# Kernel optimization log

Measured on AMD Instinct MI355X. Metric: run time of the kernel, lower is better.

The kernel has to match this reference:

```python
import jax, jax.numpy as jnp
import numpy as np

D_MODEL = 1024
NUM_HEADS = 16
HEAD_DIM = D_MODEL // NUM_HEADS
B, S = 2, 2048


def setup_inputs() -> dict:
    key = jax.random.key(0)
    ks = jax.random.split(key, 6)
    scale = 0.02
    return {
        "x": jax.random.normal(ks[0], (B, S, D_MODEL), dtype=jnp.float32),
        "mask": jax.random.normal(ks[1], (S, S), dtype=jnp.float32),
        "Wqkv": jax.random.normal(ks[2], (D_MODEL, 3 * D_MODEL), dtype=jnp.float32) * scale,
        "bqkv": jax.random.normal(ks[3], (3 * D_MODEL,), dtype=jnp.float32) * scale,
        "Wout": jax.random.normal(ks[4], (D_MODEL, D_MODEL), dtype=jnp.float32) * scale,
        "bout": jax.random.normal(ks[5], (D_MODEL,), dtype=jnp.float32) * scale,
    }


def reference(x, mask, Wqkv, bqkv, Wout, bout):
    b, s, d = x.shape
    h, hd = NUM_HEADS, HEAD_DIM
    qkv = x @ Wqkv + bqkv                              # [b, s, 3d]
    qkv = qkv.reshape(b, s, h, 3 * hd).transpose(0, 2, 1, 3)  # [b, h, s, 3hd]
    q, k, v = jnp.split(qkv, 3, axis=-1)               # each [b, h, s, hd]
    scaled = jnp.einsum("bhqd,bhkd->bhqk", q, k) / jnp.sqrt(jnp.float32(hd))
    scaled = scaled + mask                             # mask [s, s] broadcasts
    attn = jax.nn.softmax(scaled, axis=-1)
    values = jnp.einsum("bhqk,bhkd->bhqd", attn, v)    # [b, h, s, hd]
    values = values.transpose(0, 2, 1, 3).reshape(b, s, d)
    return values @ Wout + bout
```

## Files before the change

### kernel.cpp

```cpp
#include <hip/hip_runtime.h>
#include <hip/hip_bf16.h>

#define D_MODEL 1024
#define NH 16
#define HD 64
#define BATCH 2
#define SEQ 2048
#define M_TOTAL (BATCH*SEQ)

typedef _Float16 f16;
typedef _Float16 half8 __attribute__((ext_vector_type(8)));
typedef _Float16 half4v __attribute__((ext_vector_type(4)));
typedef float floatx4 __attribute__((ext_vector_type(4)));

__device__ inline void gload_lds16(const void* g, void* l) {
    __builtin_amdgcn_global_load_lds(
        (const __attribute__((address_space(1))) unsigned int*)g,
        (__attribute__((address_space(3))) unsigned int*)l, 16, 0, 0);
}

__global__ void cvt_f32_f16(const float* __restrict__ src, f16* __restrict__ dst, int n4) {
    int i = blockIdx.x * blockDim.x + threadIdx.x;
    if (i < n4) {
        float4 v = ((const float4*)src)[i];
        half4v o = { (f16)v.x, (f16)v.y, (f16)v.z, (f16)v.w };
        *(half4v*)(dst + (long)i * 4) = o;
    }
}

__global__ void exp_cvt(const float* __restrict__ src, f16* __restrict__ dst, int n4) {
    int i = blockIdx.x * blockDim.x + threadIdx.x;
    if (i < n4) {
        float4 v = ((const float4*)src)[i];
        half4v o = { (f16)__expf(v.x), (f16)__expf(v.y), (f16)__expf(v.z), (f16)__expf(v.w) };
        *(half4v*)(dst + (long)i * 4) = o;
    }
}

__global__ void transpose_cvt(const float* __restrict__ src, f16* __restrict__ dst, int R, int C) {
    __shared__ float tile[32][33];
    int tx = threadIdx.x;
    int ty = threadIdx.y;
    int c0 = blockIdx.x * 32;
    int r0 = blockIdx.y * 32;
    for (int yy = 0; yy < 32; yy += 8)
        tile[ty + yy][tx] = src[(long)(r0 + ty + yy) * C + c0 + tx];
    __syncthreads();
    for (int yy = 0; yy < 32; yy += 8)
        dst[(long)(c0 + ty + yy) * R + r0 + tx] = (f16)tile[tx][ty + yy];
}

template<int MODE, int TN>
__global__ __launch_bounds__(256) void gemm_mfma(
    const f16* __restrict__ A, const f16* __restrict__ BT,
    const float* __restrict__ bias,
    f16* __restrict__ Qh, f16* __restrict__ Kh, f16* __restrict__ Vtg,
    float* __restrict__ out, int Kdim)
{
    constexpr int NF = TN / 32;
    __shared__ f16 Ah[128 * 64];
    __shared__ f16 Bh[TN * 64];
    int tid  = threadIdx.x;
    int wid  = tid >> 6;
    int lane = tid & 63;
    int quad = lane >> 4;
    int l16  = lane & 15;
    int m0 = blockIdx.y * 128;
    int n0 = blockIdx.x * TN;
    int mrow = (wid >> 1) * 64;
    int ncol = (wid & 1) * (TN / 2);
    int grow = lane >> 3;
    int gchunk = (lane & 7) ^ (grow & 7);
    int sw0 = ((quad)     ^ (l16 & 7)) * 8;
    int sw1 = ((quad + 4) ^ (l16 & 7)) * 8;

    floatx4 acc[4][NF];
    #pragma unroll
    for (int mb = 0; mb < 4; mb++)
        #pragma unroll
        for (int nb = 0; nb < NF; nb++) acc[mb][nb] = (floatx4){0.f, 0.f, 0.f, 0.f};

    const f16* Abase = A + (long)m0 * Kdim;
    const f16* Bbase = BT + (long)n0 * Kdim;

    for (int k0 = 0; k0 < Kdim; k0 += 64) {
        #pragma unroll
        for (int j = 0; j < 4; j++) {
            int r = j * 32 + wid * 8 + grow;
            gload_lds16(Abase + (long)r * Kdim + k0 + gchunk * 8, &Ah[(j * 32 + wid * 8) * 64]);
        }
        #pragma unroll
        for (int j = 0; j < TN / 32; j++) {
            int r = j * 32 + wid * 8 + grow;
            gload_lds16(Bbase + (long)r * Kdim + k0 + gchunk * 8, &Bh[(j * 32 + wid * 8) * 64]);
        }
        __syncthreads();
        #pragma unroll
        for (int h = 0; h < 2; h++) {
            int sw = h ? sw1 : sw0;
            half8 af[4];
            #pragma unroll
            for (int mb = 0; mb < 4; mb++)
                af[mb] = *(const half8*)&Ah[(mrow + mb * 16 + l16) * 64 + sw];
            #pragma unroll
            for (int nb = 0; nb < NF; nb++) {
                half8 bf = *(const half8*)&Bh[(ncol + nb * 16 + l16) * 64 + sw];
                #pragma unroll
                for (int mb = 0; mb < 4; mb++)
                    acc[mb][nb] = __builtin_amdgcn_mfma_f32_16x16x32_f16(af[mb], bf, acc[mb][nb], 0, 0, 0);
            }
        }
        __syncthreads();
    }

    #pragma unroll
    for (int nb = 0; nb < NF; nb++) {
        int n = n0 + ncol + nb * 16 + l16;
        float bv = bias[n];
        int head = 0, t = 0, d = 0;
        if (MODE == 0) { head = n / 192; int rem = n % 192; t = rem / 64; d = rem % 64; }
        #pragma unroll
        for (int mb = 0; mb < 4; mb++) {
            int mbase = m0 + mrow + mb * 16 + quad * 4;
            if (MODE == 0) {
                int b = mbase >> 11;
                int s = mbase & 2047;
                long bh = b * NH + head;
                if (t == 2) {
                    half4v pack;
                    #pragma unroll
                    for (int r = 0; r < 4; r++) pack[r] = (f16)(acc[mb][nb][r] + bv);
                    *(half4v*)&Vtg[(bh * HD + d) * SEQ + s] = pack;
                } else if (t == 0) {
                    #pragma unroll
                    for (int r = 0; r < 4; r++)
                        Qh[(bh * SEQ + s + r) * HD + d] = (f16)((acc[mb][nb][r] + bv) * 0.125f);
                } else {
                    #pragma unroll
                    for (int r = 0; r < 4; r++)
                        Kh[(bh * SEQ + s + r) * HD + d] = (f16)(acc[mb][nb][r] + bv);
                }
            } else {
                #pragma unroll
                for (int r = 0; r < 4; r++)
                    out[(long)(mbase + r) * D_MODEL + n] = acc[mb][nb][r] + bv;
            }
        }
    }
}

__global__ __launch_bounds__(512) void attn(
    const f16* __restrict__ Qh, const f16* __restrict__ Kh, const f16* __restrict__ Vtg,
    const f16* __restrict__ E, f16* __restrict__ valh)
{
    __shared__ f16 Kl[2][64 * 64];
    __shared__ f16 Vt[2][64 * 64];
    __shared__ f16 Pl[8][16 * 68];
    int tid  = threadIdx.x;
    int wid  = tid >> 6;
    int lane = tid & 63;
    int quad = lane >> 4;
    int l16  = lane & 15;
    int bh = blockIdx.y;
    int b  = bh >> 4;
    int h  = bh & 15;
    int qblk = blockIdx.x * 128;
    int q0 = qblk + wid * 16;

    int wrow = wid * 8 + (lane >> 3);
    int kchunk = (lane & 7) ^ (wrow & 7);
    int sw0 = ((quad)     ^ (l16 & 7)) * 8;
    int sw1 = ((quad + 4) ^ (l16 & 7)) * 8;

    const f16* Qbase = Qh + ((long)bh * SEQ + q0) * HD;
    half8 qf[2];
    #pragma unroll
    for (int c = 0; c < 2; c++)
        qf[c] = *(const half8*)&Qbase[(long)l16 * HD + c * 32 + quad * 8];

    floatx4 Of[4];
    float sums[4];
    #pragma unroll
    for (int nb = 0; nb < 4; nb++) Of[nb] = (floatx4){0.f, 0.f, 0.f, 0.f};
    #pragma unroll
    for (int r = 0; r < 4; r++) sums[r] = 0.f;

    const f16* Kb = Kh + (long)bh * SEQ * HD;
    const f16* Vb = Vtg + (long)bh * HD * SEQ;
    const f16* Eb = E + (long)qblk * SEQ;

    auto stage = [&](int buf, int k0) {
        gload_lds16(Kb + (long)(k0 + wrow) * HD + kchunk * 8, &Kl[buf][(wid * 8) * 64]);
        gload_lds16(Vb + (long)wrow * SEQ + k0 + kchunk * 8, &Vt[buf][(wid * 8) * 64]);
    };
    auto loadE = [&](f16 (&ef)[4][4], int k0) {
        #pragma unroll
        for (int r = 0; r < 4; r++) {
            const f16* Erow = Eb + (long)(wid * 16 + quad * 4 + r) * SEQ + k0 + l16;
            #pragma unroll
            for (int kb = 0; kb < 4; kb++) ef[r][kb] = Erow[kb * 16];
        }
    };

    f16 efA[4][4], efB[4][4];
    stage(0, 0);
    loadE(efA, 0);
    __syncthreads();

    auto iter = [&](const int buf, f16 (&efC)[4][4], f16 (&efN)[4][4], int k0) {
        bool notlast = (k0 + 64 < SEQ);
        if (notlast) stage(buf ^ 1, k0 + 64);

        floatx4 sc[4];
        #pragma unroll
        for (int kb = 0; kb < 4; kb++) {
            half8 kf0 = *(const half8*)&Kl[buf][(kb * 16 + l16) * 64 + sw0];
            half8 kf1 = *(const half8*)&Kl[buf][(kb * 16 + l16) * 64 + sw1];
            floatx4 s = (floatx4){0.f, 0.f, 0.f, 0.f};
            s = __builtin_amdgcn_mfma_f32_16x16x32_f16(qf[0], kf0, s, 0, 0, 0);
            s = __builtin_amdgcn_mfma_f32_16x16x32_f16(qf[1], kf1, s, 0, 0, 0);
            sc[kb] = s;
        }

        #pragma unroll
        for (int kb = 0; kb < 4; kb++)
            #pragma unroll
            for (int r = 0; r < 4; r++) {
                float p = (float)efC[r][kb] * __expf(sc[kb][r]);
                sums[r] += p;
                Pl[wid][(quad * 4 + r) * 68 + kb * 16 + l16] = (f16)p;
            }

        if (notlast) loadE(efN, k0 + 64);

        half8 pf0 = *(const half8*)&Pl[wid][l16 * 68 + quad * 8];
        half8 pf1 = *(const half8*)&Pl[wid][l16 * 68 + 32 + quad * 8];

        #pragma unroll
        for (int nb = 0; nb < 4; nb++) {
            half8 vf0 = *(const half8*)&Vt[buf][(nb * 16 + l16) * 64 + sw0];
            half8 vf1 = *(const half8*)&Vt[buf][(nb * 16 + l16) * 64 + sw1];
            Of[nb] = __builtin_amdgcn_mfma_f32_16x16x32_f16(pf0, vf0, Of[nb], 0, 0, 0);
            Of[nb] = __builtin_amdgcn_mfma_f32_16x16x32_f16(pf1, vf1, Of[nb], 0, 0, 0);
        }

        __syncthreads();
    };

    for (int k0 = 0; k0 < SEQ; k0 += 128) {
        iter(0, efA, efB, k0);
        iter(1, efB, efA, k0 + 64);
    }

    float rinv[4];
    #pragma unroll
    for (int r = 0; r < 4; r++) {
        float s = sums[r];
        s += __shfl_xor(s, 1);
        s += __shfl_xor(s, 2);
        s += __shfl_xor(s, 4);
        s += __shfl_xor(s, 8);
        rinv[r] = 1.f / s;
    }

    #pragma unroll
    for (int nb = 0; nb < 4; nb++)
        #pragma unroll
        for (int r = 0; r < 4; r++) {
            int q = q0 + quad * 4 + r;
            int d = nb * 16 + l16;
            valh[((long)(b * SEQ + q)) * D_MODEL + h * HD + d] = (f16)(Of[nb][r] * rinv[r]);
        }
}

extern "C" void kernel_launch(void* const* d_in, const int* in_sizes, int n_in,
                              void* d_out, int out_size, void* d_ws, size_t ws_size,
                              hipStream_t stream) {
    const float* x    = (const float*)d_in[0];
    const float* mask = (const float*)d_in[1];
    const float* Wqkv = (const float*)d_in[2];
    const float* bqkv = (const float*)d_in[3];
    const float* Wout = (const float*)d_in[4];
    const float* bout = (const float*)d_in[5];
    float* out = (float*)d_out;

    char* ws = (char*)d_ws;
    f16* xh    = (f16*)(ws + 0);
    f16* E     = (f16*)(ws + 0);
    f16* WqkvT = (f16*)(ws + 8388608);
    f16* WoutT = (f16*)(ws + 14680064);
    f16* Qh    = (f16*)(ws + 16777216);
    f16* Kh    = (f16*)(ws + 25165824);
    f16* Vtg   = (f16*)(ws + 33554432);
    f16* valh  = (f16*)(ws + 41943040);

    cvt_f32_f16<<<4096, 256, 0, stream>>>(x, xh, M_TOTAL * D_MODEL / 4);
    transpose_cvt<<<dim3(96, 32), dim3(32, 8), 0, stream>>>(Wqkv, WqkvT, 1024, 3072);
    transpose_cvt<<<dim3(32, 32), dim3(32, 8), 0, stream>>>(Wout, WoutT, 1024, 1024);
    gemm_mfma<0, 128><<<dim3(24, 32), 256, 0, stream>>>(xh, WqkvT, bqkv, Qh, Kh, Vtg, nullptr, 1024);
    exp_cvt<<<4096, 256, 0, stream>>>(mask, E, SEQ * SEQ / 4);
    attn<<<dim3(16, 32), 512, 0, stream>>>(Qh, Kh, Vtg, E, valh);
    gemm_mfma<1, 64><<<dim3(16, 32), 256, 0, stream>>>(valh, WoutT, bout, nullptr, nullptr, nullptr, out, 1024);
}
```

Measured before the change: 219.7 us.

## Fold mask into exp2 argument, sum rows via MFMA, remap blocks per XCD

```diff
diff --git a/kernel.cpp b/kernel.cpp
--- a/kernel.cpp
+++ b/kernel.cpp
@@ -13,6 +13,12 @@
 typedef _Float16 half4v __attribute__((ext_vector_type(4)));
 typedef float floatx4 __attribute__((ext_vector_type(4)));
 
+#if __has_builtin(__builtin_amdgcn_exp2f)
+#define EXP2(x) __builtin_amdgcn_exp2f(x)
+#else
+#define EXP2(x) __expf(0.6931471805599453f * (x))
+#endif
+
 __device__ inline void gload_lds16(const void* g, void* l) {
     __builtin_amdgcn_global_load_lds(
         (const __attribute__((address_space(1))) unsigned int*)g,
@@ -28,11 +34,12 @@
     }
 }
 
-__global__ void exp_cvt(const float* __restrict__ src, f16* __restrict__ dst, int n4) {
+__global__ void l2scale_cvt(const float* __restrict__ src, f16* __restrict__ dst, int n4) {
     int i = blockIdx.x * blockDim.x + threadIdx.x;
     if (i < n4) {
         float4 v = ((const float4*)src)[i];
-        half4v o = { (f16)__expf(v.x), (f16)__expf(v.y), (f16)__expf(v.z), (f16)__expf(v.w) };
+        const float L2E = 1.44269504f;
+        half4v o = { (f16)(v.x * L2E), (f16)(v.y * L2E), (f16)(v.z * L2E), (f16)(v.w * L2E) };
         *(half4v*)(dst + (long)i * 4) = o;
     }
 }
@@ -134,7 +141,7 @@
                 } else if (t == 0) {
                     #pragma unroll
                     for (int r = 0; r < 4; r++)
-                        Qh[(bh * SEQ + s + r) * HD + d] = (f16)((acc[mb][nb][r] + bv) * 0.125f);
+                        Qh[(bh * SEQ + s + r) * HD + d] = (f16)((acc[mb][nb][r] + bv) * 0.18033688f);
                 } else {
                     #pragma unroll
                     for (int r = 0; r < 4; r++)
@@ -161,10 +168,15 @@
     int lane = tid & 63;
     int quad = lane >> 4;
     int l16  = lane & 15;
-    int bh = blockIdx.y;
+
+    int id   = blockIdx.y * 16 + blockIdx.x;
+    int xcd  = id & 7;
+    int slot = id >> 3;
+    int bh   = ((xcd & 3) << 3) | (slot >> 3);
+    int qx   = ((xcd >> 2) << 3) | (slot & 7);
     int b  = bh >> 4;
     int h  = bh & 15;
-    int qblk = blockIdx.x * 128;
+    int qblk = qx * 128;
     int q0 = qblk + wid * 16;
 
     int wrow = wid * 8 + (lane >> 3);
@@ -178,12 +190,14 @@
     for (int c = 0; c < 2; c++)
         qf[c] = *(const half8*)&Qbase[(long)l16 * HD + c * 32 + quad * 8];
 
+    half8 onesv;
+    #pragma unroll
+    for (int j = 0; j < 8; j++) onesv[j] = (f16)1.0f;
+
     floatx4 Of[4];
-    float sums[4];
+    floatx4 ssum = (floatx4){0.f, 0.f, 0.f, 0.f};
     #pragma unroll
     for (int nb = 0; nb < 4; nb++) Of[nb] = (floatx4){0.f, 0.f, 0.f, 0.f};
-    #pragma unroll
-    for (int r = 0; r < 4; r++) sums[r] = 0.f;
 
     const f16* Kb = Kh + (long)bh * SEQ * HD;
     const f16* Vb = Vtg + (long)bh * HD * SEQ;
@@ -193,25 +207,24 @@
         gload_lds16(Kb + (long)(k0 + wrow) * HD + kchunk * 8, &Kl[buf][(wid * 8) * 64]);
         gload_lds16(Vb + (long)wrow * SEQ + k0 + kchunk * 8, &Vt[buf][(wid * 8) * 64]);
     };
-    auto loadE = [&](f16 (&ef)[4][4], int k0) {
+
+    stage(0, 0);
+    __syncthreads();
+
+    auto iter = [&](const int buf, int k0) {
+        bool notlast = (k0 + 64 < SEQ);
+        if (notlast) stage(buf ^ 1, k0 + 64);
+
+        f16 ef[4][4];
         #pragma unroll
         for (int r = 0; r < 4; r++) {
             const f16* Erow = Eb + (long)(wid * 16 + quad * 4 + r) * SEQ + k0 + l16;
             #pragma unroll
             for (int kb = 0; kb < 4; kb++) ef[r][kb] = Erow[kb * 16];
         }
-    };
-
-    f16 efA[4][4], efB[4][4];
-    stage(0, 0);
-    loadE(efA, 0);
-    __syncthreads();
-
-    auto iter = [&](const int buf, f16 (&efC)[4][4], f16 (&efN)[4][4], int k0) {
-        bool notlast = (k0 + 64 < SEQ);
-        if (notlast) stage(buf ^ 1, k0 + 64);
 
         floatx4 sc[4];
+        __builtin_amdgcn_s_setprio(1);
         #pragma unroll
         for (int kb = 0; kb < 4; kb++) {
             half8 kf0 = *(const half8*)&Kl[buf][(kb * 16 + l16) * 64 + sw0];
@@ -221,21 +234,22 @@
             s = __builtin_amdgcn_mfma_f32_16x16x32_f16(qf[1], kf1, s, 0, 0, 0);
             sc[kb] = s;
         }
+        __builtin_amdgcn_s_setprio(0);
 
         #pragma unroll
         for (int kb = 0; kb < 4; kb++)
             #pragma unroll
             for (int r = 0; r < 4; r++) {
-                float p = (float)efC[r][kb] * __expf(sc[kb][r]);
-                sums[r] += p;
+                float p = EXP2(sc[kb][r] + (float)ef[r][kb]);
                 Pl[wid][(quad * 4 + r) * 68 + kb * 16 + l16] = (f16)p;
             }
 
-        if (notlast) loadE(efN, k0 + 64);
-
         half8 pf0 = *(const half8*)&Pl[wid][l16 * 68 + quad * 8];
         half8 pf1 = *(const half8*)&Pl[wid][l16 * 68 + 32 + quad * 8];
 
+        __builtin_amdgcn_s_setprio(1);
+        ssum = __builtin_amdgcn_mfma_f32_16x16x32_f16(pf0, onesv, ssum, 0, 0, 0);
+        ssum = __builtin_amdgcn_mfma_f32_16x16x32_f16(pf1, onesv, ssum, 0, 0, 0);
         #pragma unroll
         for (int nb = 0; nb < 4; nb++) {
             half8 vf0 = *(const half8*)&Vt[buf][(nb * 16 + l16) * 64 + sw0];
@@ -243,25 +257,19 @@
             Of[nb] = __builtin_amdgcn_mfma_f32_16x16x32_f16(pf0, vf0, Of[nb], 0, 0, 0);
             Of[nb] = __builtin_amdgcn_mfma_f32_16x16x32_f16(pf1, vf1, Of[nb], 0, 0, 0);
         }
+        __builtin_amdgcn_s_setprio(0);
 
         __syncthreads();
     };
 
     for (int k0 = 0; k0 < SEQ; k0 += 128) {
-        iter(0, efA, efB, k0);
-        iter(1, efB, efA, k0 + 64);
+        iter(0, k0);
+        iter(1, k0 + 64);
     }
 
     float rinv[4];
     #pragma unroll
-    for (int r = 0; r < 4; r++) {
-        float s = sums[r];
-        s += __shfl_xor(s, 1);
-        s += __shfl_xor(s, 2);
-        s += __shfl_xor(s, 4);
-        s += __shfl_xor(s, 8);
-        rinv[r] = 1.f / s;
-    }
+    for (int r = 0; r < 4; r++) rinv[r] = 1.f / ssum[r];
 
     #pragma unroll
     for (int nb = 0; nb < 4; nb++)
@@ -298,7 +306,7 @@
     transpose_cvt<<<dim3(96, 32), dim3(32, 8), 0, stream>>>(Wqkv, WqkvT, 1024, 3072);
     transpose_cvt<<<dim3(32, 32), dim3(32, 8), 0, stream>>>(Wout, WoutT, 1024, 1024);
     gemm_mfma<0, 128><<<dim3(24, 32), 256, 0, stream>>>(xh, WqkvT, bqkv, Qh, Kh, Vtg, nullptr, 1024);
-    exp_cvt<<<4096, 256, 0, stream>>>(mask, E, SEQ * SEQ / 4);
+    l2scale_cvt<<<4096, 256, 0, stream>>>(mask, E, SEQ * SEQ / 4);
     attn<<<dim3(16, 32), 512, 0, stream>>>(Qh, Kh, Vtg, E, valh);
     gemm_mfma<1, 64><<<dim3(16, 32), 256, 0, stream>>>(valh, WoutT, bout, nullptr, nullptr, nullptr, out, 1024);
 }
```

New measurement: 220.5 us. Within noise of the previous version (+0.4%).
